# Kernel tuning notes

Measured on AMD Instinct MI355X. Metric: run time of the kernel, lower is better.

The kernel has to match this reference:

```python
import jax, jax.numpy as jnp
import numpy as np

N, E = 20000, 320000
F_IN, HID, HEADS, LABELS = 128, 32, 4, 64
NEG_SLOPE = 0.2


def _layer_params(key, f_in, f_out, heads):
    k1, k2, k3 = jax.random.split(key, 3)
    s = 1.0 / np.sqrt(f_in)
    W = jax.random.normal(k1, (f_in, heads * f_out), jnp.float32) * s
    a_s = jax.random.normal(k2, (heads, f_out), jnp.float32) * s
    a_d = jax.random.normal(k3, (heads, f_out), jnp.float32) * s
    b = jnp.zeros((heads * f_out,), jnp.float32)
    return W, a_s, a_d, b


def setup_inputs() -> dict:
    key = jax.random.key(0)
    ks = jax.random.split(key, 12)
    inp = {
        "x_1": jax.random.normal(ks[0], (N, F_IN), jnp.float32),
        "edge_index_1": jax.random.randint(ks[1], (2, E), 0, N),
        "x_2": jax.random.normal(ks[2], (N, F_IN), jnp.float32),
        "edge_index_2": jax.random.randint(ks[3], (2, E), 0, N),
    }
    dims = [(F_IN, HID, HEADS), (HEADS * HID, HID, HEADS), (HEADS * HID, HID, HEADS), (HEADS * HID, LABELS, 1)]
    i = 4
    for b in (1, 2):
        for l, (fi, fo, h) in enumerate(dims, start=1):
            W, a_s, a_d, bias = _layer_params(ks[i], fi, fo, h)
            i += 1
            inp[f"W{l}_{b}"] = W
            inp[f"as{l}_{b}"] = a_s
            inp[f"ad{l}_{b}"] = a_d
            inp[f"b{l}_{b}"] = bias
    return inp


def _segment_softmax(e, seg, n):
    # numerically-stable softmax over edges grouped by destination node
    m = jax.ops.segment_max(e, seg, num_segments=n)
    ex = jnp.exp(e - m[seg])
    s = jax.ops.segment_sum(ex, seg, num_segments=n)
    return ex / s[seg]


def _gat(x, src, dst, n, W, a_s, a_d, b):
    # PyG GATConv: h = xW; e_ij = LeakyReLU(a_s.h_i + a_d.h_j); softmax over in-edges of dst; scatter-add
    heads, f_out = a_s.shape
    h = (x @ W).reshape(n, heads, f_out)            # [N,H,C]
    e = jax.nn.leaky_relu((h * a_s).sum(-1)[src] + (h * a_d).sum(-1)[dst], NEG_SLOPE)  # [E,H]
    alpha = _segment_softmax(e, dst, n)             # [E,H]
    out = jax.ops.segment_sum(h[src] * alpha[:, :, None], dst, num_segments=n)  # [N,H,C]
    return out.reshape(n, heads * f_out) + b


def _branch(x, ei, layers):
    n = x.shape[0]
    loop = jnp.arange(n)
    # add_self_loops=True (PyG default)
    src = jnp.concatenate([ei[0], loop])
    dst = jnp.concatenate([ei[1], loop])
    for i, (W, a_s, a_d, b) in enumerate(layers):
        x = _gat(x, src, dst, n, W, a_s, a_d, b)
        if i < len(layers) - 1:
            x = jax.nn.relu(x)  # dropout p=0.1 is identity at inference
    return x


def reference(x_1, edge_index_1, x_2, edge_index_2,
              W1_1, as1_1, ad1_1, b1_1, W2_1, as2_1, ad2_1, b2_1,
              W3_1, as3_1, ad3_1, b3_1, W4_1, as4_1, ad4_1, b4_1,
              W1_2, as1_2, ad1_2, b1_2, W2_2, as2_2, ad2_2, b2_2,
              W3_2, as3_2, ad3_2, b3_2, W4_2, as4_2, ad4_2, b4_2):
    l1 = [(W1_1, as1_1, ad1_1, b1_1), (W2_1, as2_1, ad2_1, b2_1),
          (W3_1, as3_1, ad3_1, b3_1), (W4_1, as4_1, ad4_1, b4_1)]
    l2 = [(W1_2, as1_2, ad1_2, b1_2), (W2_2, as2_2, ad2_2, b2_2),
          (W3_2, as3_2, ad3_2, b3_2), (W4_2, as4_2, ad4_2, b4_2)]
    o1 = _branch(x_1, edge_index_1, l1)
    o2 = _branch(x_2, edge_index_2, l2)
    return (jax.nn.sigmoid(o1) + jax.nn.sigmoid(o2)) * 0.5
```

## Files before the change

### kernel.cpp

```cpp
#include <hip/hip_runtime.h>
#include <hip/hip_fp16.h>
#include <math.h>


#define WAVE 64
#define NBKP 320

typedef _Float16 f16;
typedef f16 f16x8 __attribute__((ext_vector_type(8)));
typedef f16 f16x4 __attribute__((ext_vector_type(4)));
typedef float f32x4 __attribute__((ext_vector_type(4)));

__global__ __launch_bounds__(256) void bucket_count(
        const int* __restrict__ ei0, const int* __restrict__ ei1,
        int* __restrict__ carr, int nbuk, int E, int tot) {
    __shared__ int h[NBKP];
    int br = blockIdx.y;
    const int* ei = br ? ei1 : ei0;
    for (int i = threadIdx.x; i < NBKP; i += 256) h[i] = 0;
    __syncthreads();
    for (int t = blockIdx.x * 256 + threadIdx.x; t < tot; t += 256 * 256) {
        int dst = (t < E) ? ei[E + t] : (t - E);
        atomicAdd(&h[dst >> 6], 1);
    }
    __syncthreads();
    int* c = carr + ((size_t)br * gridDim.x + blockIdx.x) * NBKP;
    for (int i = threadIdx.x; i < NBKP; i += 256) c[i] = h[i];
}

__global__ __launch_bounds__(256) void bucket_scan1(
        int* __restrict__ carr, int* __restrict__ btot, int nblk) {
    __shared__ int smem[256];
    int br = blockIdx.y, k = blockIdx.x;
    size_t idx = ((size_t)br * nblk + threadIdx.x) * NBKP + k;
    int v = carr[idx];
    smem[threadIdx.x] = v;
    __syncthreads();
    #pragma unroll
    for (int off = 1; off < 256; off <<= 1) {
        int t = (threadIdx.x >= off) ? smem[threadIdx.x - off] : 0;
        __syncthreads();
        smem[threadIdx.x] += t;
        __syncthreads();
    }
    carr[idx] = smem[threadIdx.x] - v;
    if (threadIdx.x == 255) btot[br * NBKP + k] = smem[255];
}

__global__ __launch_bounds__(512) void bucket_scan2(
        const int* __restrict__ btot, int* __restrict__ bbase, int nbuk) {
    __shared__ int smem[512];
    int br = blockIdx.y;
    int v = (threadIdx.x < nbuk) ? btot[br * NBKP + threadIdx.x] : 0;
    smem[threadIdx.x] = v;
    __syncthreads();
    #pragma unroll
    for (int off = 1; off < 512; off <<= 1) {
        int t = (threadIdx.x >= off) ? smem[threadIdx.x - off] : 0;
        __syncthreads();
        smem[threadIdx.x] += t;
        __syncthreads();
    }
    int* bb = bbase + br * (nbuk + 1);
    if (threadIdx.x < nbuk) bb[threadIdx.x] = smem[threadIdx.x] - v;
    if (threadIdx.x == nbuk - 1) bb[nbuk] = smem[threadIdx.x];
}

__global__ __launch_bounds__(256) void bucket_scatter(
        const int* __restrict__ ei0, const int* __restrict__ ei1,
        const int* __restrict__ carr, const int* __restrict__ bbase,
        long long* __restrict__ pbuf, int nbuk, int E, int tot) {
    __shared__ int base_s[NBKP];
    __shared__ int h[NBKP];
    int br = blockIdx.y;
    const int* ei = br ? ei1 : ei0;
    const int* offb = carr + ((size_t)br * gridDim.x + blockIdx.x) * NBKP;
    const int* bb = bbase + br * (nbuk + 1);
    long long* pb = pbuf + (size_t)br * tot;
    for (int i = threadIdx.x; i < NBKP; i += 256) {
        h[i] = 0;
        base_s[i] = (i < nbuk) ? (bb[i] + offb[i]) : 0;
    }
    __syncthreads();
    for (int t = blockIdx.x * 256 + threadIdx.x; t < tot; t += 256 * 256) {
        int src, dst;
        if (t < E) { src = ei[t]; dst = ei[E + t]; }
        else       { src = dst = t - E; }
        int k = dst >> 6;
        int r = atomicAdd(&h[k], 1);
        pb[base_s[k] + r] = ((long long)dst << 32) | (unsigned)src;
    }
}

__global__ __launch_bounds__(256) void bucket_finalize(
        const long long* __restrict__ pbuf, const int* __restrict__ bbase,
        int* __restrict__ rowptrb, int* __restrict__ csrb,
        int n, int nbuk, int tot, int np) {
    __shared__ int h64[64], excl[64], cur[64];
    int br = blockIdx.y, k = blockIdx.x;
    const int* bb = bbase + br * (nbuk + 1);
    const long long* pb = pbuf + (size_t)br * tot;
    int base = bb[k], endb = bb[k + 1], cnt = endb - base;
    int* rp = rowptrb + (size_t)br * np;
    int* cs = csrb + (size_t)br * tot;
    int d0 = k << 6;
    int nn = min(64, n - d0);
    if (threadIdx.x < 64) h64[threadIdx.x] = 0;
    __syncthreads();
    for (int i = threadIdx.x; i < cnt; i += 256) {
        int dst = (int)(pb[base + i] >> 32);
        atomicAdd(&h64[dst & 63], 1);
    }
    __syncthreads();
    if (threadIdx.x == 0) {
        int run = 0;
        for (int j = 0; j < 64; ++j) { excl[j] = run; run += h64[j]; }
    }
    __syncthreads();
    if (threadIdx.x < 64) cur[threadIdx.x] = excl[threadIdx.x];
    if (threadIdx.x < nn) rp[d0 + threadIdx.x] = base + excl[threadIdx.x];
    if (k == nbuk - 1 && threadIdx.x == 64) rp[n] = endb;
    __syncthreads();
    for (int i = threadIdx.x; i < cnt; i += 256) {
        long long p = pb[base + i];
        int dst = (int)(p >> 32), src = (int)(p & 0xffffffffLL);
        int slot = atomicAdd(&cur[dst & 63], 1);
        cs[base + slot] = src;
    }
}

struct WsdArgs {
    const float* W[8];
    const float* as[8];
    const float* ad[8];
};

__global__ __launch_bounds__(256) void wsd_all(WsdArgs a, f16* __restrict__ wsd) {
    int l = blockIdx.z, b = blockIdx.y;
    int fout = (l == 3) ? 64 : 128;
    int H    = (l == 3) ? 1 : 4;
    int C    = (l == 3) ? 64 : 32;
    const float* W   = a.W[l * 2 + b];
    const float* a_s = a.as[l * 2 + b];
    const float* a_d = a.ad[l * 2 + b];
    f16* out = wsd + ((size_t)(l * 2 + b)) * 16 * 128;
    int k = blockIdx.x * 16 + (threadIdx.x & 15);
    int sc = threadIdx.x >> 4;
    float sum = 0.f;
    if (sc < 2 * H) {
        int hd = (sc < H) ? sc : sc - H;
        const float* av = (sc < H) ? a_s : a_d;
        const float4* Wr = (const float4*)(W + (size_t)k * fout + hd * C);
        const float4* ar = (const float4*)(av + hd * C);
        for (int c = 0; c < (C >> 2); ++c) {
            float4 wv = Wr[c]; float4 a4 = ar[c];
            sum += wv.x * a4.x + wv.y * a4.y + wv.z * a4.z + wv.w * a4.w;
        }
    }
    out[sc * 128 + k] = (f16)sum;
}

template <typename XT>
__global__ __launch_bounds__(256) void gemm_mfma(
        const XT* __restrict__ x0, const XT* __restrict__ x1,
        const float* __restrict__ W0, const float* __restrict__ W1,
        const f16* __restrict__ wsd,
        f16* __restrict__ hb, float* __restrict__ ssb, float* __restrict__ sdb,
        int n, int fout, int H) {
    __shared__ f16 xl[64 * 136];
    __shared__ f16 wl[80 * 136];
    int b = blockIdx.z;
    const XT* x = b ? x1 : x0;
    const float* W = b ? W1 : W0;
    f16* h = hb + (size_t)b * n * 128;
    float* ss = ssb + (size_t)b * n * 4;
    float* sd = sdb + (size_t)b * n * 4;
    int colbase = blockIdx.y * 64;
    bool last = (blockIdx.y == gridDim.y - 1);
    int lane = threadIdx.x & 63, w = threadIdx.x >> 6;

    {
        int c = threadIdx.x & 63, kb = (threadIdx.x >> 6) * 32;
        #pragma unroll 8
        for (int j = 0; j < 32; ++j)
            wl[c * 136 + kb + j] = (f16)W[(size_t)(kb + j) * fout + colbase + c];
    }
    if (last) {
        int c = threadIdx.x & 15, kb = (threadIdx.x >> 4) * 8;
        *(f16x8*)&wl[(64 + c) * 136 + kb] =
            *(const f16x8*)&wsd[(size_t)b * 2048 + c * 128 + kb];
    }
    __syncthreads();

    f16x8 B[5][4];
    #pragma unroll
    for (int ct = 0; ct < 5; ++ct)
        #pragma unroll
        for (int kc = 0; kc < 4; ++kc)
            B[ct][kc] = *(const f16x8*)
                &wl[(ct * 16 + (lane & 15)) * 136 + kc * 32 + (lane >> 4) * 8];

    for (int base = blockIdx.x * 64; base < n; base += gridDim.x * 64) {
        __syncthreads();
        {
            int r = threadIdx.x >> 2, k0 = (threadIdx.x & 3) * 32;
            int row = base + r;
            if (row < n) {
                if constexpr (sizeof(XT) == 4) {
                    const float4* x4 = (const float4*)x;
                    #pragma unroll
                    for (int j = 0; j < 8; ++j) {
                        float4 v = x4[(size_t)row * 32 + (k0 >> 2) + j];
                        f16x4 hv = {(f16)v.x, (f16)v.y, (f16)v.z, (f16)v.w};
                        *(f16x4*)&xl[r * 136 + k0 + 4 * j] = hv;
                    }
                } else {
                    const f16x8* x8 = (const f16x8*)x;
                    #pragma unroll
                    for (int j = 0; j < 4; ++j)
                        *(f16x8*)&xl[r * 136 + k0 + 8 * j] =
                            x8[(size_t)row * 16 + (k0 >> 3) + j];
                }
            } else {
                f16x4 z = {(f16)0.f, (f16)0.f, (f16)0.f, (f16)0.f};
                #pragma unroll
                for (int j = 0; j < 8; ++j)
                    *(f16x4*)&xl[r * 136 + k0 + 4 * j] = z;
            }
        }
        __syncthreads();

        f16x8 A[4];
        #pragma unroll
        for (int kc = 0; kc < 4; ++kc)
            A[kc] = *(const f16x8*)
                &xl[(w * 16 + (lane & 15)) * 136 + kc * 32 + (lane >> 4) * 8];

        f32x4 acc[5];
        #pragma unroll
        for (int ct = 0; ct < 5; ++ct) acc[ct] = (f32x4){0.f, 0.f, 0.f, 0.f};
        #pragma unroll
        for (int ct = 0; ct < 5; ++ct)
            #pragma unroll
            for (int kc = 0; kc < 4; ++kc)
                acc[ct] = __builtin_amdgcn_mfma_f32_16x16x32_f16(
                    A[kc], B[ct][kc], acc[ct], 0, 0, 0);

        int r0 = base + w * 16 + (lane >> 4) * 4;
        int c0 = lane & 15;
        #pragma unroll
        for (int ct = 0; ct < 4; ++ct) {
            int col = colbase + ct * 16 + c0;
            #pragma unroll
            for (int j = 0; j < 4; ++j) {
                int row = r0 + j;
                if (row < n) h[(size_t)row * fout + col] = (f16)acc[ct][j];
            }
        }
        if (last) {
            #pragma unroll
            for (int j = 0; j < 4; ++j) {
                int row = r0 + j;
                if (row < n) {
                    float v = acc[4][j];
                    if (c0 < H)          ss[(size_t)row * H + c0] = v;
                    else if (c0 < 2 * H) sd[(size_t)row * H + c0 - H] = v;
                }
            }
        }
    }
}

__global__ __launch_bounds__(256) void gather128_f(
        const __half2* __restrict__ h2, const float* __restrict__ ss,
        const float* __restrict__ sd, const int* __restrict__ rowptr,
        const int* __restrict__ csr, const float* __restrict__ bias,
        f16* __restrict__ out, int n) {
    int wid = threadIdx.x >> 6, lane = threadIdx.x & 63;
    int v = blockIdx.x * 4 + wid;
    if (v >= n) return;
    int beg = rowptr[v], end = rowptr[v + 1];
    int hd = lane >> 4;
    int sub = lane & 15;
    int hd16 = hd * 16;
    float sd_h = sd[v * 4 + hd];

    float acc0 = 0.f, acc1 = 0.f, den = 0.f;
    int i0 = beg;
    for (; i0 + 16 <= end; i0 += 16) {
        int myidx = csr[i0 + sub];
        float sc = ss[myidx * 4 + hd] + sd_h;
        sc = fmaxf(sc, 0.2f * sc);
        float w_reg = __expf(sc);
        unsigned hv[16];
        #pragma unroll
        for (int j = 0; j < 16; ++j) {
            int s = __shfl(myidx, j);
            hv[j] = *(const unsigned*)&h2[s * 64 + lane];
        }
        #pragma unroll
        for (int j = 0; j < 16; ++j) {
            float w = __shfl(w_reg, hd16 + j);
            float2 f = __half22float2(*(const __half2*)&hv[j]);
            acc0 = fmaf(w, f.x, acc0);
            acc1 = fmaf(w, f.y, acc1);
            den += w;
        }
    }
    int rem = end - i0;
    if (rem > 0) {
        int myidx = (sub < rem) ? csr[i0 + sub] : -1;
        float w_reg = 0.f;
        if (myidx >= 0) {
            float sc = ss[myidx * 4 + hd] + sd_h;
            sc = fmaxf(sc, 0.2f * sc);
            w_reg = __expf(sc);
        }
        #pragma unroll 4
        for (int j = 0; j < rem; ++j) {
            int s = __shfl(myidx, j);
            float w = __shfl(w_reg, hd16 + j);
            float2 f = __half22float2(h2[s * 64 + lane]);
            acc0 = fmaf(w, f.x, acc0);
            acc1 = fmaf(w, f.y, acc1);
            den += w;
        }
    }

    float inv = 1.f / den;
    float2 b2 = ((const float2*)bias)[lane];
    float o0 = fmaxf(fmaf(acc0, inv, b2.x), 0.f);
    float o1 = fmaxf(fmaf(acc1, inv, b2.y), 0.f);
    __half2 ov = __floats2half2_rn(o0, o1);
    __builtin_nontemporal_store(*(unsigned int*)&ov,
                                (unsigned int*)&out[v * 128 + 2 * lane]);
}

__global__ __launch_bounds__(256) void gather64_both(
        const __half* __restrict__ h0, const __half* __restrict__ h1,
        const float* __restrict__ ss0, const float* __restrict__ ss1,
        const float* __restrict__ sd0, const float* __restrict__ sd1,
        const int* __restrict__ rp0, const int* __restrict__ rp1,
        const int* __restrict__ csr0, const int* __restrict__ csr1,
        const float* __restrict__ bias0, const float* __restrict__ bias1,
        float* __restrict__ out, int n) {
    int wid = threadIdx.x >> 6, lane = threadIdx.x & 63;
    int v = blockIdx.x * 4 + wid;
    if (v >= n) return;
    int sub = lane & 15;
    float og = 0.f;

    #pragma unroll
    for (int br = 0; br < 2; ++br) {
        const __half* h   = br ? h1 : h0;
        const float* ss   = br ? ss1 : ss0;
        const float* sd   = br ? sd1 : sd0;
        const int* rowptr = br ? rp1 : rp0;
        const int* csr    = br ? csr1 : csr0;
        const float* bias = br ? bias1 : bias0;
        int beg = rowptr[v], end = rowptr[v + 1];
        float sd_v = sd[v];
        float acc = 0.f, den = 0.f;
        int i0 = beg;
        for (; i0 + 16 <= end; i0 += 16) {
            int myidx = csr[i0 + sub];
            float sc = ss[myidx] + sd_v;
            sc = fmaxf(sc, 0.2f * sc);
            float w_reg = __expf(sc);
            unsigned short hv[16];
            #pragma unroll
            for (int j = 0; j < 16; ++j) {
                int s = __shfl(myidx, j);
                hv[j] = *(const unsigned short*)&h[s * 64 + lane];
            }
            #pragma unroll
            for (int j = 0; j < 16; ++j) {
                float w = __shfl(w_reg, j);
                float f = __half2float(*(const __half*)&hv[j]);
                acc = fmaf(w, f, acc);
                den += w;
            }
        }
        int rem = end - i0;
        if (rem > 0) {
            int myidx = (sub < rem) ? csr[i0 + sub] : -1;
            float w_reg = 0.f;
            if (myidx >= 0) {
                float sc = ss[myidx] + sd_v;
                sc = fmaxf(sc, 0.2f * sc);
                w_reg = __expf(sc);
            }
            #pragma unroll 4
            for (int j = 0; j < rem; ++j) {
                int s = __shfl(myidx, j);
                float w = __shfl(w_reg, j);
                float f = __half2float(h[s * 64 + lane]);
                acc = fmaf(w, f, acc);
                den += w;
            }
        }
        float o = acc / den + bias[lane];
        og += 0.5f / (1.f + __expf(-o));
    }
    out[(size_t)v * 64 + lane] = og;
}

extern "C" void kernel_launch(void* const* d_in, const int* in_sizes, int n_in,
                              void* d_out, int out_size, void* d_ws, size_t ws_size,
                              hipStream_t stream) {
    const int N = in_sizes[0] / 128;
    const int E = in_sizes[1] / 2;
    const int TOT = E + N;
    const int NP = N + 4;
    const int NBUK = (N + 63) >> 6;
    const int NBLK = 256;

    const float* x1 = (const float*)d_in[0];
    const int*   ei1 = (const int*)d_in[1];
    const float* x2 = (const float*)d_in[2];
    const int*   ei2 = (const int*)d_in[3];
    void* const* P0 = d_in + 4;
    void* const* P1 = d_in + 20;

    char* w = (char*)d_ws;
    f16* bufX = (f16*)w;               w += (size_t)2 * N * 128 * 2;
    f16* bufH = (f16*)w;               w += (size_t)2 * N * 128 * 2;
    float* s_src = (float*)w;          w += (size_t)2 * N * 4 * 4;
    float* s_dst = (float*)w;          w += (size_t)2 * N * 4 * 4;
    int* rowptr = (int*)w;             w += (size_t)2 * NP * 4;
    int* csr_src = (int*)w;            w += (size_t)2 * TOT * 4;
    int* carr = (int*)w;               w += (size_t)2 * NBLK * NBKP * 4;
    int* btot = (int*)w;               w += (size_t)2 * NBKP * 4;
    int* bbase = (int*)w;              w += (size_t)2 * (NBUK + 1) * 4 + 8;
    long long* pbuf = (long long*)w;   w += (size_t)2 * TOT * 8;
    f16* wsd = (f16*)w;                w += (size_t)8 * 2048 * 2;

    dim3 blk(256);
    int gWave  = (N + 3) / 4;

    WsdArgs wa;
    for (int l = 0; l < 4; ++l) {
        int o = (l < 3) ? l * 4 : 12;
        wa.W[l * 2 + 0]  = (const float*)P0[o + 0];
        wa.W[l * 2 + 1]  = (const float*)P1[o + 0];
        wa.as[l * 2 + 0] = (const float*)P0[o + 1];
        wa.as[l * 2 + 1] = (const float*)P1[o + 1];
        wa.ad[l * 2 + 0] = (const float*)P0[o + 2];
        wa.ad[l * 2 + 1] = (const float*)P1[o + 2];
    }
    wsd_all<<<dim3(8, 2, 4), blk, 0, stream>>>(wa, wsd);

    bucket_count<<<dim3(NBLK, 2), blk, 0, stream>>>(ei1, ei2, carr, NBUK, E, TOT);
    bucket_scan1<<<dim3(NBUK, 2), blk, 0, stream>>>(carr, btot, NBLK);
    bucket_scan2<<<dim3(1, 2), dim3(512), 0, stream>>>(btot, bbase, NBUK);
    bucket_scatter<<<dim3(NBLK, 2), blk, 0, stream>>>(ei1, ei2, carr, bbase,
                                                      pbuf, NBUK, E, TOT);
    bucket_finalize<<<dim3(NBUK, 2), blk, 0, stream>>>(pbuf, bbase, rowptr,
                                                       csr_src, N, NBUK, TOT, NP);

    for (int l = 0; l < 3; ++l) {
        if (l == 0)
            gemm_mfma<float><<<dim3(128, 2, 2), blk, 0, stream>>>(
                x1, x2,
                (const float*)P0[0], (const float*)P1[0],
                wsd + (size_t)l * 4096, bufH, s_src, s_dst, N, 128, 4);
        else
            gemm_mfma<f16><<<dim3(128, 2, 2), blk, 0, stream>>>(
                bufX, bufX + (size_t)N * 128,
                (const float*)P0[l*4+0], (const float*)P1[l*4+0],
                wsd + (size_t)l * 4096, bufH, s_src, s_dst, N, 128, 4);
        for (int b = 0; b < 2; ++b)
            gather128_f<<<gWave, blk, 0, stream>>>(
                (const __half2*)(bufH + (size_t)b * N * 128),
                s_src + (size_t)b * N * 4, s_dst + (size_t)b * N * 4,
                rowptr + (size_t)b * NP, csr_src + (size_t)b * TOT,
                (const float*)(b ? P1[l*4+3] : P0[l*4+3]),
                bufX + (size_t)b * N * 128, N);
    }

    gemm_mfma<f16><<<dim3(128, 1, 2), blk, 0, stream>>>(
        bufX, bufX + (size_t)N * 128,
        (const float*)P0[12], (const float*)P1[12],
        wsd + (size_t)3 * 4096, bufH, s_src, s_dst, N, 64, 1);
    gather64_both<<<gWave, blk, 0, stream>>>(
        (const __half*)bufH, (const __half*)(bufH + (size_t)N * 128),
        s_src, s_src + (size_t)N * 4, s_dst, s_dst + (size_t)N * 4,
        rowptr, rowptr + NP, csr_src, csr_src + (size_t)TOT,
        (const float*)P0[15], (const float*)P1[15],
        (float*)d_out, N);
}
```

Before: 238.2 us.

## Process two nodes per wavefront in gather and vectorize GEMM output stores

```diff
diff --git a/kernel.cpp b/kernel.cpp
--- a/kernel.cpp
+++ b/kernel.cpp
@@ -244,27 +244,23 @@
             #pragma unroll
             for (int kc = 0; kc < 4; ++kc)
                 acc[ct] = __builtin_amdgcn_mfma_f32_16x16x32_f16(
-                    A[kc], B[ct][kc], acc[ct], 0, 0, 0);
-
-        int r0 = base + w * 16 + (lane >> 4) * 4;
-        int c0 = lane & 15;
-        #pragma unroll
-        for (int ct = 0; ct < 4; ++ct) {
-            int col = colbase + ct * 16 + c0;
+                    B[ct][kc], A[kc], acc[ct], 0, 0, 0);
+
+        int xrow = base + w * 16 + (lane & 15);
+        int cg = lane >> 4;
+        if (xrow < n) {
             #pragma unroll
-            for (int j = 0; j < 4; ++j) {
-                int row = r0 + j;
-                if (row < n) h[(size_t)row * fout + col] = (f16)acc[ct][j];
-            }
-        }
-        if (last) {
-            #pragma unroll
-            for (int j = 0; j < 4; ++j) {
-                int row = r0 + j;
-                if (row < n) {
-                    float v = acc[4][j];
-                    if (c0 < H)          ss[(size_t)row * H + c0] = v;
-                    else if (c0 < 2 * H) sd[(size_t)row * H + c0 - H] = v;
+            for (int ct = 0; ct < 4; ++ct) {
+                f16x4 hv = {(f16)acc[ct][0], (f16)acc[ct][1],
+                            (f16)acc[ct][2], (f16)acc[ct][3]};
+                *(f16x4*)&h[(size_t)xrow * fout + colbase + ct * 16 + cg * 4] = hv;
+            }
+            if (last) {
+                if (H == 4) {
+                    if (cg == 0)      *(float4*)&ss[(size_t)xrow * 4] = *(float4*)&acc[4];
+                    else if (cg == 1) *(float4*)&sd[(size_t)xrow * 4] = *(float4*)&acc[4];
+                } else {
+                    if (cg == 0) { ss[xrow] = acc[4][0]; sd[xrow] = acc[4][1]; }
                 }
             }
         }
@@ -277,63 +273,131 @@
         const int* __restrict__ csr, const float* __restrict__ bias,
         f16* __restrict__ out, int n) {
     int wid = threadIdx.x >> 6, lane = threadIdx.x & 63;
-    int v = blockIdx.x * 4 + wid;
-    if (v >= n) return;
-    int beg = rowptr[v], end = rowptr[v + 1];
-    int hd = lane >> 4;
-    int sub = lane & 15;
-    int hd16 = hd * 16;
-    float sd_h = sd[v * 4 + hd];
-
-    float acc0 = 0.f, acc1 = 0.f, den = 0.f;
-    int i0 = beg;
-    for (; i0 + 16 <= end; i0 += 16) {
-        int myidx = csr[i0 + sub];
-        float sc = ss[myidx * 4 + hd] + sd_h;
-        sc = fmaxf(sc, 0.2f * sc);
-        float w_reg = __expf(sc);
-        unsigned hv[16];
-        #pragma unroll
-        for (int j = 0; j < 16; ++j) {
-            int s = __shfl(myidx, j);
-            hv[j] = *(const unsigned*)&h2[s * 64 + lane];
-        }
-        #pragma unroll
-        for (int j = 0; j < 16; ++j) {
-            float w = __shfl(w_reg, hd16 + j);
-            float2 f = __half22float2(*(const __half2*)&hv[j]);
-            acc0 = fmaf(w, f.x, acc0);
-            acc1 = fmaf(w, f.y, acc1);
-            den += w;
-        }
-    }
-    int rem = end - i0;
-    if (rem > 0) {
-        int myidx = (sub < rem) ? csr[i0 + sub] : -1;
-        float w_reg = 0.f;
-        if (myidx >= 0) {
-            float sc = ss[myidx * 4 + hd] + sd_h;
-            sc = fmaxf(sc, 0.2f * sc);
-            w_reg = __expf(sc);
+    int jw = blockIdx.x * 4 + wid;
+    int v0 = 2 * jw, v1 = v0 + 1;
+    if (v0 >= n) return;
+    bool has1 = (v1 < n);
+    int hd = lane >> 4, sub = lane & 15, hd16 = hd * 16;
+
+    int beg0 = rowptr[v0], end0 = rowptr[v0 + 1];
+    int beg1 = has1 ? rowptr[v1] : 0, end1 = has1 ? rowptr[v1 + 1] : 0;
+    float sdh0 = sd[v0 * 4 + hd];
+    float sdh1 = has1 ? sd[v1 * 4 + hd] : 0.f;
+
+    float a00 = 0.f, a01 = 0.f, d0 = 0.f;
+    float a10 = 0.f, a11 = 0.f, d1 = 0.f;
+    int i0 = beg0, i1 = beg1;
+
+    for (; i0 + 16 <= end0 && i1 + 16 <= end1; i0 += 16, i1 += 16) {
+        int idx0 = csr[i0 + sub];
+        int idx1 = csr[i1 + sub];
+        float sc0 = ss[idx0 * 4 + hd] + sdh0; sc0 = fmaxf(sc0, 0.2f * sc0);
+        float sc1 = ss[idx1 * 4 + hd] + sdh1; sc1 = fmaxf(sc1, 0.2f * sc1);
+        float w0 = __expf(sc0), w1 = __expf(sc1);
+        unsigned hv0[16], hv1[16];
+        #pragma unroll
+        for (int j = 0; j < 16; ++j) {
+            int s = __shfl(idx0, j);
+            hv0[j] = *(const unsigned*)&h2[s * 64 + lane];
+        }
+        #pragma unroll
+        for (int j = 0; j < 16; ++j) {
+            int s = __shfl(idx1, j);
+            hv1[j] = *(const unsigned*)&h2[s * 64 + lane];
+        }
+        #pragma unroll
+        for (int j = 0; j < 16; ++j) {
+            float w = __shfl(w0, hd16 + j);
+            float2 f = __half22float2(*(const __half2*)&hv0[j]);
+            a00 = fmaf(w, f.x, a00); a01 = fmaf(w, f.y, a01); d0 += w;
+        }
+        #pragma unroll
+        for (int j = 0; j < 16; ++j) {
+            float w = __shfl(w1, hd16 + j);
+            float2 f = __half22float2(*(const __half2*)&hv1[j]);
+            a10 = fmaf(w, f.x, a10); a11 = fmaf(w, f.y, a11); d1 += w;
+        }
+    }
+    for (; i0 + 16 <= end0; i0 += 16) {
+        int idx0 = csr[i0 + sub];
+        float sc0 = ss[idx0 * 4 + hd] + sdh0; sc0 = fmaxf(sc0, 0.2f * sc0);
+        float w0 = __expf(sc0);
+        unsigned hv0[16];
+        #pragma unroll
+        for (int j = 0; j < 16; ++j) {
+            int s = __shfl(idx0, j);
+            hv0[j] = *(const unsigned*)&h2[s * 64 + lane];
+        }
+        #pragma unroll
+        for (int j = 0; j < 16; ++j) {
+            float w = __shfl(w0, hd16 + j);
+            float2 f = __half22float2(*(const __half2*)&hv0[j]);
+            a00 = fmaf(w, f.x, a00); a01 = fmaf(w, f.y, a01); d0 += w;
+        }
+    }
+    for (; i1 + 16 <= end1; i1 += 16) {
+        int idx1 = csr[i1 + sub];
+        float sc1 = ss[idx1 * 4 + hd] + sdh1; sc1 = fmaxf(sc1, 0.2f * sc1);
+        float w1 = __expf(sc1);
+        unsigned hv1[16];
+        #pragma unroll
+        for (int j = 0; j < 16; ++j) {
+            int s = __shfl(idx1, j);
+            hv1[j] = *(const unsigned*)&h2[s * 64 + lane];
+        }
+        #pragma unroll
+        for (int j = 0; j < 16; ++j) {
+            float w = __shfl(w1, hd16 + j);
+            float2 f = __half22float2(*(const __half2*)&hv1[j]);
+            a10 = fmaf(w, f.x, a10); a11 = fmaf(w, f.y, a11); d1 += w;
+        }
+    }
+    {
+        int rem0 = end0 - i0, rem1 = end1 - i1;
+        int idx0 = (sub < rem0) ? csr[i0 + sub] : -1;
+        int idx1 = (sub < rem1) ? csr[i1 + sub] : -1;
+        float w0 = 0.f, w1 = 0.f;
+        if (idx0 >= 0) {
+            float sc = ss[idx0 * 4 + hd] + sdh0; sc = fmaxf(sc, 0.2f * sc);
+            w0 = __expf(sc);
+        }
+        if (idx1 >= 0) {
+            float sc = ss[idx1 * 4 + hd] + sdh1; sc = fmaxf(sc, 0.2f * sc);
+            w1 = __expf(sc);
         }
         #pragma unroll 4
-        for (int j = 0; j < rem; ++j) {
-            int s = __shfl(myidx, j);
-            float w = __shfl(w_reg, hd16 + j);
+        for (int j = 0; j < rem0; ++j) {
+            int s = __shfl(idx0, j);
+            float w = __shfl(w0, hd16 + j);
             float2 f = __half22float2(h2[s * 64 + lane]);
-            acc0 = fmaf(w, f.x, acc0);
-            acc1 = fmaf(w, f.y, acc1);
-            den += w;
-        }
-    }
-
-    float inv = 1.f / den;
+            a00 = fmaf(w, f.x, a00); a01 = fmaf(w, f.y, a01); d0 += w;
+        }
+        #pragma unroll 4
+        for (int j = 0; j < rem1; ++j) {
+            int s = __shfl(idx1, j);
+            float w = __shfl(w1, hd16 + j);
+            float2 f = __half22float2(h2[s * 64 + lane]);
+            a10 = fmaf(w, f.x, a10); a11 = fmaf(w, f.y, a11); d1 += w;
+        }
+    }
+
     float2 b2 = ((const float2*)bias)[lane];
-    float o0 = fmaxf(fmaf(acc0, inv, b2.x), 0.f);
-    float o1 = fmaxf(fmaf(acc1, inv, b2.y), 0.f);
-    __half2 ov = __floats2half2_rn(o0, o1);
-    __builtin_nontemporal_store(*(unsigned int*)&ov,
-                                (unsigned int*)&out[v * 128 + 2 * lane]);
+    {
+        float inv = 1.f / d0;
+        float o0 = fmaxf(fmaf(a00, inv, b2.x), 0.f);
+        float o1 = fmaxf(fmaf(a01, inv, b2.y), 0.f);
+        __half2 ov = __floats2half2_rn(o0, o1);
+        __builtin_nontemporal_store(*(unsigned int*)&ov,
+                                    (unsigned int*)&out[v0 * 128 + 2 * lane]);
+    }
+    if (has1) {
+        float inv = 1.f / d1;
+        float o0 = fmaxf(fmaf(a10, inv, b2.x), 0.f);
+        float o1 = fmaxf(fmaf(a11, inv, b2.y), 0.f);
+        __half2 ov = __floats2half2_rn(o0, o1);
+        __builtin_nontemporal_store(*(unsigned int*)&ov,
+                                    (unsigned int*)&out[v1 * 128 + 2 * lane]);
+    }
 }
 
 __global__ __launch_bounds__(256) void gather64_both(
@@ -437,6 +501,7 @@
 
     dim3 blk(256);
     int gWave  = (N + 3) / 4;
+    int gWave2 = ((N + 1) / 2 + 3) / 4;
 
     WsdArgs wa;
     for (int l = 0; l < 4; ++l) {
@@ -470,7 +535,7 @@
                 (const float*)P0[l*4+0], (const float*)P1[l*4+0],
                 wsd + (size_t)l * 4096, bufH, s_src, s_dst, N, 128, 4);
         for (int b = 0; b < 2; ++b)
-            gather128_f<<<gWave, blk, 0, stream>>>(
+            gather128_f<<<gWave2, blk, 0, stream>>>(
                 (const __half2*)(bufH + (size_t)b * N * 128),
                 s_src + (size_t)b * N * 4, s_dst + (size_t)b * N * 4,
                 rowptr + (size_t)b * NP, csr_src + (size_t)b * TOT,
```

New measurement: 294.2 us. 1.24x slower.

## Split each node's edge gather across two wavefronts and reduce through LDS

Applied to the files above, without the earlier changes.

```diff
diff --git a/kernel.cpp b/kernel.cpp
--- a/kernel.cpp
+++ b/kernel.cpp
@@ -276,64 +276,74 @@
         const float* __restrict__ sd, const int* __restrict__ rowptr,
         const int* __restrict__ csr, const float* __restrict__ bias,
         f16* __restrict__ out, int n) {
+    __shared__ float r0s[4][64], r1s[4][64], rds[4][64];
     int wid = threadIdx.x >> 6, lane = threadIdx.x & 63;
-    int v = blockIdx.x * 4 + wid;
-    if (v >= n) return;
-    int beg = rowptr[v], end = rowptr[v + 1];
+    int pair = wid >> 1, half = wid & 1;
+    int v = blockIdx.x * 2 + pair;
+    bool valid = (v < n);
     int hd = lane >> 4;
     int sub = lane & 15;
     int hd16 = hd * 16;
-    float sd_h = sd[v * 4 + hd];
 
     float acc0 = 0.f, acc1 = 0.f, den = 0.f;
-    int i0 = beg;
-    for (; i0 + 16 <= end; i0 += 16) {
-        int myidx = csr[i0 + sub];
-        float sc = ss[myidx * 4 + hd] + sd_h;
-        sc = fmaxf(sc, 0.2f * sc);
-        float w_reg = __expf(sc);
-        unsigned hv[16];
-        #pragma unroll
-        for (int j = 0; j < 16; ++j) {
-            int s = __shfl(myidx, j);
-            hv[j] = *(const unsigned*)&h2[s * 64 + lane];
-        }
-        #pragma unroll
-        for (int j = 0; j < 16; ++j) {
-            float w = __shfl(w_reg, hd16 + j);
-            float2 f = __half22float2(*(const __half2*)&hv[j]);
-            acc0 = fmaf(w, f.x, acc0);
-            acc1 = fmaf(w, f.y, acc1);
-            den += w;
-        }
-    }
-    int rem = end - i0;
-    if (rem > 0) {
-        int myidx = (sub < rem) ? csr[i0 + sub] : -1;
-        float w_reg = 0.f;
-        if (myidx >= 0) {
+    if (valid) {
+        int beg = rowptr[v], end = rowptr[v + 1];
+        float sd_h = sd[v * 4 + hd];
+        int i0 = beg + half * 16;
+        for (; i0 + 16 <= end; i0 += 32) {
+            int myidx = csr[i0 + sub];
             float sc = ss[myidx * 4 + hd] + sd_h;
             sc = fmaxf(sc, 0.2f * sc);
-            w_reg = __expf(sc);
-        }
-        #pragma unroll 4
-        for (int j = 0; j < rem; ++j) {
-            int s = __shfl(myidx, j);
-            float w = __shfl(w_reg, hd16 + j);
-            float2 f = __half22float2(h2[s * 64 + lane]);
-            acc0 = fmaf(w, f.x, acc0);
-            acc1 = fmaf(w, f.y, acc1);
-            den += w;
-        }
-    }
-
-    float inv = 1.f / den;
-    float2 b2 = ((const float2*)bias)[lane];
-    float o0 = fmaxf(fmaf(acc0, inv, b2.x), 0.f);
-    float o1 = fmaxf(fmaf(acc1, inv, b2.y), 0.f);
-    __half2 ov = __floats2half2_rn(o0, o1);
-    __builtin_nontemporal_store(*(unsigned int*)&ov,
-                                (unsigned int*)&out[v * 128 + 2 * lane]);
+            float w_reg = __expf(sc);
+            unsigned hv[16];
+            #pragma unroll
+            for (int j = 0; j < 16; ++j) {
+                int s = __shfl(myidx, j);
+                hv[j] = *(const unsigned*)&h2[s * 64 + lane];
+            }
+            #pragma unroll
+            for (int j = 0; j < 16; ++j) {
+                float w = __shfl(w_reg, hd16 + j);
+                float2 f = __half22float2(*(const __half2*)&hv[j]);
+                acc0 = fmaf(w, f.x, acc0);
+                acc1 = fmaf(w, f.y, acc1);
+                den += w;
+            }
+        }
+        int rem = end - i0;
+        if (rem > 0) {
+            int myidx = (sub < rem) ? csr[i0 + sub] : -1;
+            float w_reg = 0.f;
+            if (myidx >= 0) {
+                float sc = ss[myidx * 4 + hd] + sd_h;
+                sc = fmaxf(sc, 0.2f * sc);
+                w_reg = __expf(sc);
+            }
+            #pragma unroll 4
+            for (int j = 0; j < rem; ++j) {
+                int s = __shfl(myidx, j);
+                float w = __shfl(w_reg, hd16 + j);
+                float2 f = __half22float2(h2[s * 64 + lane]);
+                acc0 = fmaf(w, f.x, acc0);
+                acc1 = fmaf(w, f.y, acc1);
+                den += w;
+            }
+        }
+    }
+    r0s[wid][lane] = acc0; r1s[wid][lane] = acc1; rds[wid][lane] = den;
+    __syncthreads();
+    if (half == 0 && valid) {
+        acc0 += r0s[wid + 1][lane];
+        acc1 += r1s[wid + 1][lane];
+        den  += rds[wid + 1][lane];
+        float inv = 1.f / den;
+        float2 b2 = ((const float2*)bias)[lane];
+        float o0 = fmaxf(fmaf(acc0, inv, b2.x), 0.f);
+        float o1 = fmaxf(fmaf(acc1, inv, b2.y), 0.f);
+        __half2 ov = __floats2half2_rn(o0, o1);
+        __builtin_nontemporal_store(*(unsigned int*)&ov,
+                                    (unsigned int*)&out[v * 128 + 2 * lane]);
+    }
 }
 
 __global__ __launch_bounds__(256) void gather64_both(
@@ -344,14 +354,15 @@
         const int* __restrict__ csr0, const int* __restrict__ csr1,
         const float* __restrict__ bias0, const float* __restrict__ bias1,
         float* __restrict__ out, int n) {
+    __shared__ float rsg[4][64];
     int wid = threadIdx.x >> 6, lane = threadIdx.x & 63;
-    int v = blockIdx.x * 4 + wid;
-    if (v >= n) return;
+    int pair = wid >> 1, br = wid & 1;
+    int v = blockIdx.x * 2 + pair;
+    bool valid = (v < n);
     int sub = lane & 15;
-    float og = 0.f;
-
-    #pragma unroll
-    for (int br = 0; br < 2; ++br) {
+
+    float sg = 0.f;
+    if (valid) {
         const __half* h   = br ? h1 : h0;
         const float* ss   = br ? ss1 : ss0;
         const float* sd   = br ? sd1 : sd0;
@@ -400,9 +411,12 @@
             }
         }
         float o = acc / den + bias[lane];
-        og += 0.5f / (1.f + __expf(-o));
-    }
-    out[(size_t)v * 64 + lane] = og;
+        sg = 0.5f / (1.f + __expf(-o));
+    }
+    rsg[wid][lane] = sg;
+    __syncthreads();
+    if (br == 0 && valid)
+        out[(size_t)v * 64 + lane] = sg + rsg[wid + 1][lane];
 }
 
 extern "C" void kernel_launch(void* const* d_in, const int* in_sizes, int n_in,
@@ -436,7 +450,7 @@
     f16* wsd = (f16*)w;                w += (size_t)8 * 2048 * 2;
 
     dim3 blk(256);
-    int gWave  = (N + 3) / 4;
+    int gPair = (N + 1) / 2;
 
     WsdArgs wa;
     for (int l = 0; l < 4; ++l) {
@@ -470,7 +484,7 @@
                 (const float*)P0[l*4+0], (const float*)P1[l*4+0],
                 wsd + (size_t)l * 4096, bufH, s_src, s_dst, N, 128, 4);
         for (int b = 0; b < 2; ++b)
-            gather128_f<<<gWave, blk, 0, stream>>>(
+            gather128_f<<<gPair, blk, 0, stream>>>(
                 (const __half2*)(bufH + (size_t)b * N * 128),
                 s_src + (size_t)b * N * 4, s_dst + (size_t)b * N * 4,
                 rowptr + (size_t)b * NP, csr_src + (size_t)b * TOT,
@@ -482,7 +496,7 @@
         bufX, bufX + (size_t)N * 128,
         (const float*)P0[12], (const float*)P1[12],
         wsd + (size_t)3 * 4096, bufH, s_src, s_dst, N, 64, 1);
-    gather64_both<<<gWave, blk, 0, stream>>>(
+    gather64_both<<<gPair, blk, 0, stream>>>(
         (const __half*)bufH, (const __half*)(bufH + (size_t)N * 128),
         s_src, s_src + (size_t)N * 4, s_dst, s_dst + (size_t)N * 4,
         rowptr, rowptr + NP, csr_src, csr_src + (size_t)TOT,
```

Measured after the change: 287.2 us. 1.21x slower.
